# Performance work log

Hardware: AMD Instinct MI355X
Metric: run time of the kernel (lower is better)

The kernel has to match this reference:

```python
import jax, jax.numpy as jnp
import numpy as np

CTX, SP, HIST, NC = 168, 24, 336, 128
LAGS = [24, 48, 72, 96, 120, 144, 168, 0]  # lags_seq + [0]
NSEG = CTX // SP  # 7


def gru_cell(x, h, Wih, Whh, bih, bhh):
    # torch.nn.GRUCell math; x: (N, D), h: (N, H)
    gi = x @ Wih.T + bih
    gh = h @ Whh.T + bhh
    ir, iz, inn = jnp.split(gi, 3, axis=-1)
    hr, hz, hn = jnp.split(gh, 3, axis=-1)
    r = jax.nn.sigmoid(ir + hr)
    z = jax.nn.sigmoid(iz + hz)
    n = jnp.tanh(inn + r * hn)
    return (1.0 - z) * n + z * h


def lstm(x, h, c, Wih, Whh, b):
    # single-layer batch_first LSTM; x: (B, T, D); torch gate order i,f,g,o
    xw = jnp.einsum('btd,gd->btg', x, Wih) + b  # precompute input projection
    def step(carry, xt):
        h, c = carry
        gates = xt + h @ Whh.T
        i, f, g, o = jnp.split(gates, 4, axis=-1)
        c = jax.nn.sigmoid(f) * c + jax.nn.sigmoid(i) * jnp.tanh(g)
        h = jax.nn.sigmoid(o) * jnp.tanh(c)
        return (h, c), h
    (h, c), ys = jax.lax.scan(step, (h, c), jnp.swapaxes(xw, 0, 1))
    return jnp.swapaxes(ys, 0, 1), h, c


def setup_inputs() -> dict:
    key = jax.random.key(0)
    ks = jax.random.split(key, 20)
    B = 8192
    p = lambda k, shape: jax.random.normal(k, shape, jnp.float32) * 0.05
    return dict(
        feat_static_cat=jax.random.randint(ks[0], (B, 1), 0, 50),
        feat_static_real=jax.random.normal(ks[1], (B, 1), jnp.float32),
        past_time_feat=jax.random.normal(ks[2], (B, HIST, 4), jnp.float32),
        past_target=jax.random.uniform(ks[3], (B, HIST), jnp.float32),
        past_observed_values=jnp.ones((B, HIST), jnp.float32),
        future_time_feat=jax.random.normal(ks[4], (B, SP, 4), jnp.float32),
        emb_table=p(ks[5], (50, 16)),
        gru_Wih=p(ks[6], (3 * NC, 30)),
        gru_Whh=p(ks[7], (3 * NC, NC)),
        gru_bih=p(ks[8], (3 * NC,)),
        gru_bhh=p(ks[9], (3 * NC,)),
        enc_Wih=p(ks[10], (NSEG, 4 * NC, NC)),
        enc_Whh=p(ks[11], (NSEG, 4 * NC, NC)),
        enc_b=p(ks[12], (NSEG, 4 * NC)),
        dec_Wih=p(ks[13], (4 * NC, 180)),
        dec_Whh=p(ks[14], (4 * NC, NC)),
        dec_b=p(ks[15], (4 * NC,)),
        out_W=p(ks[16], (1, NC)),
        out_b=p(ks[17], (1,)),
    )


def reference(feat_static_cat, feat_static_real, past_time_feat, past_target,
              past_observed_values, future_time_feat,
              emb_table, gru_Wih, gru_Whh, gru_bih, gru_bhh,
              enc_Wih, enc_Whh, enc_b, dec_Wih, dec_Whh, dec_b,
              out_W, out_b):
    B = past_target.shape[0]
    time_feat = past_time_feat[:, HIST - CTX:, :]  # (B, CTX, 4)

    # lagged subsequences: lagged[:, j, k] = seq[:, HIST - lag_k - CTX + j]
    lags = jnp.stack(
        [past_target[:, HIST - lag - CTX: HIST - lag] for lag in LAGS], axis=-1
    )  # (B, CTX, 8)

    # MeanScaler over past_target[:, CTX:] (keepdim)
    data = past_target[:, CTX:]
    w = past_observed_values[:, CTX:]
    total_w = w.sum(axis=1)                     # (B,)
    wsum = (jnp.abs(data) * w).sum(axis=1)      # (B,)
    default_scale = wsum.sum() / jnp.maximum(total_w.sum(), 1.0)
    scale = wsum / jnp.maximum(total_w, 1.0)
    scale = jnp.maximum(1e-10, jnp.where(wsum > 0, scale, default_scale))
    scale = scale[:, None]                      # (B, 1)

    embedded = emb_table[feat_static_cat[:, 0]]  # (B, 16)
    static_feat = jnp.concatenate([embedded, feat_static_real, jnp.log(scale)], axis=1)  # (B, 18)
    rep_static = jnp.broadcast_to(static_feat[:, None, :], (B, CTX, static_feat.shape[-1]))

    lags_scaled = lags / scale[:, :, None]
    inputs = jnp.concatenate([lags_scaled, time_feat, rep_static], axis=-1)  # (B, CTX, 30)
    inputs = inputs.reshape(B, NSEG, SP, inputs.shape[-1])  # (B, 7, 24, 30)

    encoder_out = jnp.zeros((B, SP, NC), inputs.dtype)
    h = jnp.zeros((B, NC), inputs.dtype)
    c = jnp.zeros((B, NC), inputs.dtype)
    for i in range(NSEG):  # fixed small loop; each segment has distinct LSTM weights
        x = inputs[:, i].reshape(-1, inputs.shape[-1])  # (B*SP, 30)
        hv = gru_cell(x, encoder_out.reshape(-1, NC), gru_Wih, gru_Whh, gru_bih, gru_bhh)
        hv = hv.reshape(B, SP, NC)
        encoder_out, h, c = lstm(hv, h, c, enc_Wih[i], enc_Whh[i], enc_b[i])

    query = jnp.concatenate(
        [inputs[:, 0], encoder_out, future_time_feat, rep_static[:, -SP:, :]], axis=-1
    )  # (B, 24, 180)
    dec_out, _, _ = lstm(query, h, c, dec_Wih, dec_Whh, dec_b)
    outputs = dec_out @ out_W.T + out_b  # (B, 24, 1)
    return outputs * scale[:, :, None]
```

## Files before the change

### kernel.cpp

```cpp
#include <hip/hip_runtime.h>
#include <math.h>

typedef short bf16x8 __attribute__((ext_vector_type(8)));
typedef float f32x4 __attribute__((ext_vector_type(4)));
typedef unsigned short u16;
typedef unsigned int u32;

#define WSUMS 0
#define TOTWS 1
#define WSUM_OFF 2
#define TOTW_OFF 8194
#define SCL_F 16386
#define WB_BYTE 98432

#define GWI_U 0
#define GWH_U 12288
#define EO_U  61440
#define DO_U  978944
#define XG_U  1142784
#define XD_U  23162880

#define L2E 1.4426950408889634f
#define T2E 2.8853900817779268f

__constant__ int cLAG[8] = {144,120,96,72,48,24,0,168};

__device__ __forceinline__ float sig2(float x){
  return __builtin_amdgcn_rcpf(1.0f+__builtin_amdgcn_exp2f(-x));
}
__device__ __forceinline__ float th2(float x){
  return __builtin_fmaf(-2.0f, __builtin_amdgcn_rcpf(__builtin_amdgcn_exp2f(x)+1.0f), 1.0f);
}
__device__ __forceinline__ float thc(float x){
  return th2(x*T2E);
}
__device__ __forceinline__ u16 f2b(float x){ u32 u=__float_as_uint(x); return (u16)((u + 0x7fffu + ((u>>16)&1u))>>16); }
__device__ __forceinline__ float b2f(u16 v){ return __uint_as_float(((u32)v)<<16); }
__device__ __forceinline__ u32 f2b_pk(float lo, float hi){
  u32 r; asm("v_cvt_pk_bf16_f32 %0, %1, %2" : "=v"(r) : "v"(lo), "v"(hi)); return r;
}
__device__ __forceinline__ void pin(bf16x8 &x){
  f32x4 t = __builtin_bit_cast(f32x4, x);
  asm volatile("" : "+v"(t));
  x = __builtin_bit_cast(bf16x8, t);
}

#define MFMA(a,b,c) __builtin_amdgcn_mfma_f32_16x16x32_bf16(a,b,c,0,0,0)

__global__ void scale_kernel(const float* __restrict__ tgt,
                             const float* __restrict__ obs,
                             float* __restrict__ ws)
{
  __shared__ float s1[256], s2[256];
  int b = blockIdx.x*256 + threadIdx.x;
  float wsum=0.f, totw=0.f;
  const float* tr = tgt + b*336 + 168;
  const float* wr = obs + b*336 + 168;
  for(int t=0;t<168;t++){ float w=wr[t]; wsum += fabsf(tr[t])*w; totw += w; }
  ws[WSUM_OFF + b] = wsum;
  ws[TOTW_OFF + b] = totw;
  s1[threadIdx.x]=wsum; s2[threadIdx.x]=totw;
  __syncthreads();
  for(int s=128;s>0;s>>=1){
    if(threadIdx.x<s){ s1[threadIdx.x]+=s1[threadIdx.x+s]; s2[threadIdx.x]+=s2[threadIdx.x+s]; }
    __syncthreads();
  }
  if(threadIdx.x==0){ atomicAdd(&ws[WSUMS], s1[0]); atomicAdd(&ws[TOTWS], s2[0]); }
}

__global__ void prep_w(const float* __restrict__ gWih, const float* __restrict__ gWhh,
                       const float* __restrict__ eWih, const float* __restrict__ eWhh,
                       const float* __restrict__ dWih, const float* __restrict__ dWhh,
                       float* __restrict__ ws)
{
  u16* WU = (u16*)((char*)ws + WB_BYTE);
  int tid = blockIdx.x*blockDim.x + threadIdx.x;
  int nt = gridDim.x*blockDim.x;
  for(int i=tid;i<12288;i+=nt){ int n=i>>5,k=i&31;
    float s=((n>>7)==2)?T2E:L2E;
    WU[GWI_U+i]=(k<30)?f2b(gWih[n*30+k]*s):(u16)0; }
  for(int i=tid;i<49152;i+=nt){ int n=i>>7,k=i&127;
    float s=((n>>7)==2)?T2E:L2E;
    WU[GWH_U+i]=f2b(gWhh[n*128+k]*s); }
  for(int i=tid;i<917504;i+=nt){
    int s=i>>17,r2=i&131071,n=r2>>8,k=r2&255;
    float sc=((n>>7)==2)?T2E:L2E;
    float v=(k<128)?eWih[(s*512+n)*128+k]:eWhh[(s*512+n)*128+(k-128)];
    WU[EO_U+i]=f2b(v*sc);
  }
  for(int i=tid;i<163840;i+=nt){
    int n=i/320, k=i-n*320; float v;
    float sc=((n>>7)==2)?T2E:L2E;
    if(k<128)       v=dWih[n*180+30+k];
    else if(k<136)  v=dWih[n*180+(k-128)];
    else if(k<140)  v=dWih[n*180+8+(k-136)];
    else if(k<144)  v=dWih[n*180+158+(k-140)];
    else if(k<162)  v=dWih[n*180+12+(k-144)];
    else if(k<180)  v=dWih[n*180+162+(k-162)];
    else if(k<192)  v=0.f;
    else            v=dWhh[n*128+(k-192)];
    WU[DO_U+i]=f2b(v*sc);
  }
}

__global__ void prep_x(const float* __restrict__ tgt, const float* __restrict__ ptf,
                       const float* __restrict__ ftf, float* __restrict__ ws)
{
  __shared__ float inv_l[64];
  u16* WU = (u16*)((char*)ws + WB_BYTE);
  const int tid = threadIdx.x;
  const int b0 = blockIdx.x*64;
  if(tid<64){
    int b=b0+tid;
    float wsumv=ws[WSUM_OFF+b], totw=ws[TOTW_OFF+b];
    float def=ws[WSUMS]/fmaxf(ws[TOTWS],1.f);
    float sc=fmaxf(1e-10f,(wsumv>0.f)?wsumv/fmaxf(totw,1.f):def);
    ws[SCL_F+b]=sc; inv_l[tid]=1.f/sc;
  }
  __syncthreads();
  for(int idx=tid; idx<64*168; idx+=256){
    int bl=idx/168, gt=idx-bl*168; int b=b0+bl;
    float iv=inv_l[bl];
    __align__(16) u16 row[16];
    #pragma unroll
    for(int j=0;j<8;j++) row[j]=f2b(tgt[b*336+cLAG[j]+gt]*iv);
    const float* pp=ptf+((size_t)(b*336+168+gt))*4;
    #pragma unroll
    for(int j=0;j<4;j++) row[8+j]=f2b(pp[j]);
    row[12]=row[13]=row[14]=row[15]=0;
    int seg=gt/24, t=gt-seg*24;
    u16* dst=WU+XG_U+(((size_t)seg*8192+b)*24+t)*16;
    *(uint4*)dst=*(const uint4*)row; *(uint4*)(dst+8)=*(const uint4*)(row+8);
  }
  for(int idx=tid; idx<64*24; idx+=256){
    int bl=idx/24, t=idx-bl*24; int b=b0+bl;
    float iv=inv_l[bl];
    __align__(16) u16 row[16];
    #pragma unroll
    for(int j=0;j<8;j++) row[j]=f2b(tgt[b*336+cLAG[j]+t]*iv);
    #pragma unroll
    for(int j=0;j<4;j++) row[8+j]=f2b(ptf[((size_t)(b*336+168+t))*4+j]);
    #pragma unroll
    for(int j=0;j<4;j++) row[12+j]=f2b(ftf[b*96+t*4+j]);
    u16* dst=WU+XD_U+((size_t)b*24+t)*16;
    *(uint4*)dst=*(const uint4*)row; *(uint4*)(dst+8)=*(const uint4*)(row+8);
  }
}

__global__ __launch_bounds__(512,2)
__attribute__((amdgpu_waves_per_eu(2,2)))
void deepar_main(const int* __restrict__ cat, const float* __restrict__ sreal,
                 const float* __restrict__ emb,
                 const float* __restrict__ gbih, const float* __restrict__ gbhh,
                 const float* __restrict__ encb, const float* __restrict__ decb,
                 const float* __restrict__ outW, const float* __restrict__ outb,
                 float* __restrict__ ws, float* __restrict__ out)
{
  asm volatile("" ::: "v252","v253","v254","v255");

  const u16* __restrict__ WU=(const u16*)((const char*)ws+WB_BYTE);

  __shared__ __align__(16) u16 encbuf[384*136];
  __shared__ __align__(16) u16 Ast[2][16*136];
  __shared__ __align__(16) u16 Xast[2][64*40];
  __shared__ __align__(16) u16 Xdast[16*72];
  __shared__ __align__(16) u16 hstash[2][16*136];
  __shared__ u16 statb[16][18];
  __shared__ float scl_s[16];
  __shared__ float outw_s[128];
  __shared__ float red[16][8];
  __shared__ float outb_s;

  const int tid=threadIdx.x;
  const int b0=blockIdx.x*16;
  const int wv=tid>>6, lane=tid&63, quad=lane>>4, l15=lane&15;

  auto stageX = [&](int gc){
    if(tid<128 && gc<42){
      int sg=gc/6, cc=gc-sg*6;
      int a=tid>>1;
      u16* Xb=&Xast[gc&1][0];
      const u16* src=WU+XG_U+(((size_t)sg*8192+b0+(a>>2))*24+4*cc+(a&3))*16;
      if(tid&1) *(uint2*)(Xb+a*40+8)=*(const uint2*)(src+8);
      else      *(uint4*)(Xb+a*40)  =*(const uint4*)src;
    }
  };

  if(tid<16) scl_s[tid]=ws[SCL_F+b0+tid];
  if(tid<128) outw_s[tid]=outW[tid];
  if(tid==128) outb_s=outb[0];
  if(tid>=256){ int q=tid-256; int r=q>>4,k=q&15; statb[r][k]=f2b(emb[cat[b0+r]*16+k]); }
  { const uint4 z4={0,0,0,0};
    for(int i=tid;i<6528;i+=512) *(uint4*)(encbuf+i*8)=z4;
    for(int i=tid;i<544;i+=512)  *(uint4*)(&hstash[0][0]+i*8)=z4;
  }
  __syncthreads();
  if(tid<16){ statb[tid][16]=f2b(sreal[b0+tid]); statb[tid][17]=f2b(logf(scl_s[tid])); }
  __syncthreads();
  for(int i=tid;i<1280;i+=512){ int a=i/20, k=i-a*20+12;
    u16 v=(k<30)?statb[a>>2][k-12]:(u16)0;
    Xast[0][a*40+k]=v; Xast[1][a*40+k]=v; }
  for(int i=tid;i<896;i+=512){ int rr=i/56, k=i-rr*56+16;
    u16 v; if(k<34) v=statb[rr][k-16]; else if(k<52) v=statb[rr][k-34]; else v=0;
    Xdast[rr*72+k]=v; }
  stageX(0);
  __syncthreads();

  float gbi[3], gbh[3];
  #pragma unroll
  for(int j=0;j<3;j++){ int nb=(wv+j*8)*16+l15;
    float s=(j==2)?T2E:L2E;
    gbi[j]=gbih[nb]*s; gbh[j]=gbhh[nb]*s; }
  const float gbr=gbi[0]+gbh[0], gbz=gbi[1]+gbh[1];
  const f32x4 b4r ={gbr,gbr,gbr,gbr};
  const f32x4 b4z ={gbz,gbz,gbz,gbz};
  const f32x4 b4i2={gbi[2],gbi[2],gbi[2],gbi[2]};
  const f32x4 b4h2={gbh[2],gbh[2],gbh[2],gbh[2]};

  float cst[4]={0.f,0.f,0.f,0.f};
  const int hc=wv*16+l15;
  int p=0;

  for(int seg=0;seg<7;seg++){
    bf16x8 gwi[3]; bf16x8 gwh[3][4];
    #pragma unroll
    for(int j=0;j<3;j++){
      int nb=(wv+j*8)*16+l15;
      gwi[j]=*(const bf16x8*)(WU+GWI_U+nb*32+quad*8); pin(gwi[j]);
      #pragma unroll
      for(int kt=0;kt<4;kt++){ gwh[j][kt]=*(const bf16x8*)(WU+GWH_U+nb*128+kt*32+quad*8); pin(gwh[j][kt]); }
    }

    for(int c=0;c<6;c++){
      stageX(seg*6+c+1);
      const u16* Xb = &Xast[c&1][0];

      f32x4 g01[2][4], a2[4], h2[4];
      #pragma unroll
      for(int mt=0;mt<4;mt++){
        bf16x8 af=*(const bf16x8*)(Xb+(mt*16+l15)*40+quad*8);
        g01[0][mt]=MFMA(af,gwi[0],b4r);
        g01[1][mt]=MFMA(af,gwi[1],b4z);
        a2[mt]   =MFMA(af,gwi[2],b4i2);
      }
      const u16* ebase=encbuf+(size_t)(c*64)*136;
      #pragma unroll
      for(int kt=0;kt<4;kt++)
        #pragma unroll
        for(int mt=0;mt<4;mt++){
          bf16x8 af=*(const bf16x8*)(ebase+(mt*16+l15)*136+kt*32+quad*8);
          g01[0][mt]=MFMA(af,gwh[0][kt],g01[0][mt]);
          g01[1][mt]=MFMA(af,gwh[1][kt],g01[1][mt]);
          h2[mt]   =MFMA(af,gwh[2][kt],(kt==0)?b4h2:h2[mt]);
        }
      u16 hv16[4][4];
      #pragma unroll
      for(int mt=0;mt<4;mt++){
        float hv[4];
        #pragma unroll
        for(int reg=0;reg<4;reg++){
          int a=mt*16+quad*4+reg;
          float rg=sig2(g01[0][mt][reg]);
          float zg=sig2(g01[1][mt][reg]);
          float hp=b2f(encbuf[(c*64+a)*136+hc]);
          float nn=th2(__builtin_fmaf(rg,h2[mt][reg],a2[mt][reg]));
          hv[reg]=__builtin_fmaf(zg,hp-nn,nn);
        }
        u32 p01=f2b_pk(hv[0],hv[1]), p23=f2b_pk(hv[2],hv[3]);
        hv16[mt][0]=(u16)p01; hv16[mt][1]=(u16)(p01>>16);
        hv16[mt][2]=(u16)p23; hv16[mt][3]=(u16)(p23>>16);
      }
      __syncthreads();
      #pragma unroll
      for(int mt=0;mt<4;mt++)
        #pragma unroll
        for(int reg=0;reg<4;reg++)
          encbuf[(c*64+mt*16+quad*4+reg)*136+hc]=hv16[mt][reg];
    }

    bf16x8 we[4][8]; f32x4 b4e[4];
    #pragma unroll
    for(int j=0;j<4;j++){
      int nb=(wv+j*8)*16+l15;
      float b=encb[seg*512+nb]*((j==2)?T2E:L2E);
      b4e[j]=(f32x4){b,b,b,b};
      #pragma unroll
      for(int kt=0;kt<8;kt++){
        we[j][kt]=*(const bf16x8*)(WU+EO_U+(size_t)seg*131072+nb*256+kt*32+quad*8);
        pin(we[j][kt]);
      }
    }
    for(int t=0;t<24;t++){
      int tb=(t>>2)*64+(t&3);
      u16* Ab=&Ast[t&1][0];
      if(tid<256){ int row=tid>>4,q=tid&15;
        *(uint4*)(Ab+row*136+q*8)=*(const uint4*)(encbuf+(tb+row*4)*136+q*8); }
      __syncthreads();
      const u16* Hb=&hstash[p][0];
      f32x4 acc[4];
      #pragma unroll
      for(int kt=0;kt<8;kt++){
        bf16x8 af=(kt<4)? *(const bf16x8*)(Ab+l15*136+kt*32+quad*8)
                        : *(const bf16x8*)(Hb+l15*136+(kt-4)*32+quad*8);
        #pragma unroll
        for(int j=0;j<4;j++) acc[j]=MFMA(af,we[j][kt],(kt==0)?b4e[j]:acc[j]);
      }
      u16 hnew[4];
      { float hf[4];
        #pragma unroll
        for(int reg=0;reg<4;reg++){
          float ig=sig2(acc[0][reg]),fg=sig2(acc[1][reg]);
          float gg=th2(acc[2][reg]), og=sig2(acc[3][reg]);
          float c_=__builtin_fmaf(fg,cst[reg],ig*gg); cst[reg]=c_;
          hf[reg]=og*thc(c_);
        }
        u32 p01=f2b_pk(hf[0],hf[1]), p23=f2b_pk(hf[2],hf[3]);
        hnew[0]=(u16)p01; hnew[1]=(u16)(p01>>16);
        hnew[2]=(u16)p23; hnew[3]=(u16)(p23>>16);
      }
      int pn=p^1;
      u16* Hw=&hstash[pn][0];
      #pragma unroll
      for(int reg=0;reg<4;reg++){
        int row=quad*4+reg;
        Hw[row*136+hc]=hnew[reg];
        encbuf[(tb+row*4)*136+hc]=hnew[reg];
      }
      p=pn;
    }
  }

  bf16x8 wd[4][10]; f32x4 b4d[4];
  #pragma unroll
  for(int j=0;j<4;j++){
    int nb=(wv+j*8)*16+l15;
    float b=decb[nb]*((j==2)?T2E:L2E);
    b4d[j]=(f32x4){b,b,b,b};
    #pragma unroll
    for(int kt=0;kt<10;kt++){
      wd[j][kt]=*(const bf16x8*)(WU+DO_U+nb*320+kt*32+quad*8);
      pin(wd[j][kt]);
    }
  }
  for(int t=0;t<24;t++){
    int tb=(t>>2)*64+(t&3);
    u16* Ab=&Ast[t&1][0];
    if(tid<256){ int row=tid>>4,q=tid&15;
      *(uint4*)(Ab+row*136+q*8)=*(const uint4*)(encbuf+(tb+row*4)*136+q*8); }
    else if(tid<288){ int q=tid-256; int rr=q>>1;
      const u16* src=WU+XD_U+((size_t)(b0+rr)*24+t)*16;
      if(q&1) *(uint4*)(Xdast+rr*72+8)=*(const uint4*)(src+8);
      else    *(uint4*)(Xdast+rr*72)  =*(const uint4*)src; }
    __syncthreads();
    const u16* Hb=&hstash[p][0];
    f32x4 acc[4];
    #pragma unroll
    for(int kt=0;kt<10;kt++){
      bf16x8 af=(kt<4)? *(const bf16x8*)(Ab+l15*136+kt*32+quad*8)
              :(kt<6)? *(const bf16x8*)(Xdast+l15*72+(kt-4)*32+quad*8)
                     : *(const bf16x8*)(Hb+l15*136+(kt-6)*32+quad*8);
      #pragma unroll
      for(int j=0;j<4;j++) acc[j]=MFMA(af,wd[j][kt],(kt==0)?b4d[j]:acc[j]);
    }
    u16 hnew[4];
    { float hf[4];
      #pragma unroll
      for(int reg=0;reg<4;reg++){
        float ig=sig2(acc[0][reg]),fg=sig2(acc[1][reg]);
        float gg=th2(acc[2][reg]), og=sig2(acc[3][reg]);
        float c_=__builtin_fmaf(fg,cst[reg],ig*gg); cst[reg]=c_;
        hf[reg]=og*thc(c_);
      }
      u32 p01=f2b_pk(hf[0],hf[1]), p23=f2b_pk(hf[2],hf[3]);
      hnew[0]=(u16)p01; hnew[1]=(u16)(p01>>16);
      hnew[2]=(u16)p23; hnew[3]=(u16)(p23>>16);
    }
    int pn=p^1;
    #pragma unroll
    for(int reg=0;reg<4;reg++)
      hstash[pn][(quad*4+reg)*136+hc]=hnew[reg];
    __syncthreads();
    if(tid<128){ int row=tid>>3,g=tid&7; float s=0.f;
      #pragma unroll
      for(int i=0;i<16;i++) s+=b2f(hstash[pn][row*136+g*16+i])*outw_s[g*16+i];
      red[row][g]=s; }
    __syncthreads();
    if(tid<16){ float s=outb_s;
      #pragma unroll
      for(int g=0;g<8;g++) s+=red[tid][g];
      out[(b0+tid)*24+t]=s*scl_s[tid]; }
    p=pn;
  }
}

extern "C" void kernel_launch(void* const* d_in, const int* in_sizes, int n_in,
                              void* d_out, int out_size, void* d_ws, size_t ws_size,
                              hipStream_t stream)
{
  (void)in_sizes; (void)n_in; (void)out_size; (void)ws_size;
  const int*   cat  = (const int*)d_in[0];
  const float* sreal= (const float*)d_in[1];
  const float* ptf  = (const float*)d_in[2];
  const float* tgt  = (const float*)d_in[3];
  const float* obs  = (const float*)d_in[4];
  const float* ftf  = (const float*)d_in[5];
  const float* emb  = (const float*)d_in[6];
  const float* gWih = (const float*)d_in[7];
  const float* gWhh = (const float*)d_in[8];
  const float* gbih = (const float*)d_in[9];
  const float* gbhh = (const float*)d_in[10];
  const float* eWih = (const float*)d_in[11];
  const float* eWhh = (const float*)d_in[12];
  const float* encb = (const float*)d_in[13];
  const float* dWih = (const float*)d_in[14];
  const float* dWhh = (const float*)d_in[15];
  const float* decb = (const float*)d_in[16];
  const float* outW = (const float*)d_in[17];
  const float* outb = (const float*)d_in[18];
  float* ws  = (float*)d_ws;
  float* out = (float*)d_out;

  hipMemsetAsync(d_ws, 0, 2*sizeof(float), stream);
  scale_kernel<<<dim3(8192/256), dim3(256), 0, stream>>>(tgt, obs, ws);
  prep_w<<<dim3(512), dim3(256), 0, stream>>>(gWih,gWhh,eWih,eWhh,dWih,dWhh,ws);
  prep_x<<<dim3(128), dim3(256), 0, stream>>>(tgt, ptf, ftf, ws);
  deepar_main<<<dim3(512), dim3(512), 0, stream>>>(cat,sreal,emb,gbih,gbhh,encb,decb,
                                                   outW,outb,ws,out);
}
```

Baseline: 939.2 us.

## Precompute next-step input projections and drop LDS staging copies in LSTM loops

The encoder LSTM's input-side MFMAs for step t+1 are now computed during step t, after the recurrent MFMAs, so only the hidden-state half of the product stays on the serial dependency chain. The A-operand staging buffer is removed and rows are read directly from encbuf with a strided address. In the decoder, the per-step global load of future features is double-buffered and issued one step ahead. The X staging ring grows to four slots so it can prefetch two chunks ahead. This adds register pressure from the extra accumulators and reorders the barriers, so correctness depends on the remaining syncthreads protecting hstash and encbuf.

```diff
diff --git a/kernel.cpp b/kernel.cpp
--- a/kernel.cpp
+++ b/kernel.cpp
@@ -161,9 +161,8 @@
   const u16* __restrict__ WU=(const u16*)((const char*)ws+WB_BYTE);
 
   __shared__ __align__(16) u16 encbuf[384*136];
-  __shared__ __align__(16) u16 Ast[2][16*136];
-  __shared__ __align__(16) u16 Xast[2][64*40];
-  __shared__ __align__(16) u16 Xdast[16*72];
+  __shared__ __align__(16) u16 Xast[4][64*40];
+  __shared__ __align__(16) u16 Xdast[2][16*72];
   __shared__ __align__(16) u16 hstash[2][16*136];
   __shared__ u16 statb[16][18];
   __shared__ float scl_s[16];
@@ -179,7 +178,7 @@
     if(tid<128 && gc<42){
       int sg=gc/6, cc=gc-sg*6;
       int a=tid>>1;
-      u16* Xb=&Xast[gc&1][0];
+      u16* Xb=&Xast[gc&3][0];
       const u16* src=WU+XG_U+(((size_t)sg*8192+b0+(a>>2))*24+4*cc+(a&3))*16;
       if(tid&1) *(uint2*)(Xb+a*40+8)=*(const uint2*)(src+8);
       else      *(uint4*)(Xb+a*40)  =*(const uint4*)src;
@@ -199,11 +198,11 @@
   __syncthreads();
   for(int i=tid;i<1280;i+=512){ int a=i/20, k=i-a*20+12;
     u16 v=(k<30)?statb[a>>2][k-12]:(u16)0;
-    Xast[0][a*40+k]=v; Xast[1][a*40+k]=v; }
+    Xast[0][a*40+k]=v; Xast[1][a*40+k]=v; Xast[2][a*40+k]=v; Xast[3][a*40+k]=v; }
   for(int i=tid;i<896;i+=512){ int rr=i/56, k=i-rr*56+16;
     u16 v; if(k<34) v=statb[rr][k-16]; else if(k<52) v=statb[rr][k-34]; else v=0;
-    Xdast[rr*72+k]=v; }
-  stageX(0);
+    Xdast[0][rr*72+k]=v; Xdast[1][rr*72+k]=v; }
+  stageX(0); stageX(1);
   __syncthreads();
 
   float gbi[3], gbh[3];
@@ -232,8 +231,8 @@
     }
 
     for(int c=0;c<6;c++){
-      stageX(seg*6+c+1);
-      const u16* Xb = &Xast[c&1][0];
+      stageX(seg*6+c+2);
+      const u16* Xb = &Xast[(seg*6+c)&3][0];
 
       f32x4 g01[2][4], a2[4], h2[4];
       #pragma unroll
@@ -290,20 +289,35 @@
         pin(we[j][kt]);
       }
     }
+    f32x4 accA[4];
+    {
+      const u16* Ar=encbuf+(size_t)(l15*4)*136;
+      #pragma unroll
+      for(int kt=0;kt<4;kt++){
+        bf16x8 af=*(const bf16x8*)(Ar+kt*32+quad*8);
+        #pragma unroll
+        for(int j=0;j<4;j++) accA[j]=MFMA(af,we[j][kt],(kt==0)?b4e[j]:accA[j]);
+      }
+    }
     for(int t=0;t<24;t++){
-      int tb=(t>>2)*64+(t&3);
-      u16* Ab=&Ast[t&1][0];
-      if(tid<256){ int row=tid>>4,q=tid&15;
-        *(uint4*)(Ab+row*136+q*8)=*(const uint4*)(encbuf+(tb+row*4)*136+q*8); }
       __syncthreads();
       const u16* Hb=&hstash[p][0];
       f32x4 acc[4];
       #pragma unroll
-      for(int kt=0;kt<8;kt++){
-        bf16x8 af=(kt<4)? *(const bf16x8*)(Ab+l15*136+kt*32+quad*8)
-                        : *(const bf16x8*)(Hb+l15*136+(kt-4)*32+quad*8);
-        #pragma unroll
-        for(int j=0;j<4;j++) acc[j]=MFMA(af,we[j][kt],(kt==0)?b4e[j]:acc[j]);
+      for(int kt=0;kt<4;kt++){
+        bf16x8 af=*(const bf16x8*)(Hb+l15*136+kt*32+quad*8);
+        #pragma unroll
+        for(int j=0;j<4;j++) acc[j]=MFMA(af,we[j][kt+4],(kt==0)?accA[j]:acc[j]);
+      }
+      if(t<23){
+        int tb1=((t+1)>>2)*64+((t+1)&3);
+        const u16* Ar=encbuf+(size_t)(tb1+l15*4)*136;
+        #pragma unroll
+        for(int kt=0;kt<4;kt++){
+          bf16x8 af=*(const bf16x8*)(Ar+kt*32+quad*8);
+          #pragma unroll
+          for(int j=0;j<4;j++) accA[j]=MFMA(af,we[j][kt],(kt==0)?b4e[j]:accA[j]);
+        }
       }
       u16 hnew[4];
       { float hf[4];
@@ -319,6 +333,7 @@
         hnew[2]=(u16)p23; hnew[3]=(u16)(p23>>16);
       }
       int pn=p^1;
+      int tb=(t>>2)*64+(t&3);
       u16* Hw=&hstash[pn][0];
       #pragma unroll
       for(int reg=0;reg<4;reg++){
@@ -342,26 +357,31 @@
       pin(wd[j][kt]);
     }
   }
+  if(tid>=256 && tid<288){ int q=tid-256; int rr=q>>1;
+    const u16* src=WU+XD_U+((size_t)(b0+rr)*24+0)*16;
+    u16* Xw=&Xdast[0][0];
+    if(q&1) *(uint4*)(Xw+rr*72+8)=*(const uint4*)(src+8);
+    else    *(uint4*)(Xw+rr*72)  =*(const uint4*)src; }
+  __syncthreads();
   for(int t=0;t<24;t++){
     int tb=(t>>2)*64+(t&3);
-    u16* Ab=&Ast[t&1][0];
-    if(tid<256){ int row=tid>>4,q=tid&15;
-      *(uint4*)(Ab+row*136+q*8)=*(const uint4*)(encbuf+(tb+row*4)*136+q*8); }
-    else if(tid<288){ int q=tid-256; int rr=q>>1;
-      const u16* src=WU+XD_U+((size_t)(b0+rr)*24+t)*16;
-      if(q&1) *(uint4*)(Xdast+rr*72+8)=*(const uint4*)(src+8);
-      else    *(uint4*)(Xdast+rr*72)  =*(const uint4*)src; }
-    __syncthreads();
+    const u16* Ar=encbuf+(size_t)(tb+l15*4)*136;
+    const u16* Xd=&Xdast[t&1][0];
     const u16* Hb=&hstash[p][0];
     f32x4 acc[4];
     #pragma unroll
     for(int kt=0;kt<10;kt++){
-      bf16x8 af=(kt<4)? *(const bf16x8*)(Ab+l15*136+kt*32+quad*8)
-              :(kt<6)? *(const bf16x8*)(Xdast+l15*72+(kt-4)*32+quad*8)
+      bf16x8 af=(kt<4)? *(const bf16x8*)(Ar+kt*32+quad*8)
+              :(kt<6)? *(const bf16x8*)(Xd+l15*72+(kt-4)*32+quad*8)
                      : *(const bf16x8*)(Hb+l15*136+(kt-6)*32+quad*8);
       #pragma unroll
       for(int j=0;j<4;j++) acc[j]=MFMA(af,wd[j][kt],(kt==0)?b4d[j]:acc[j]);
     }
+    if(t<23 && tid>=256 && tid<288){ int q=tid-256; int rr=q>>1;
+      const u16* src=WU+XD_U+((size_t)(b0+rr)*24+t+1)*16;
+      u16* Xw=&Xdast[(t+1)&1][0];
+      if(q&1) *(uint4*)(Xw+rr*72+8)=*(const uint4*)(src+8);
+      else    *(uint4*)(Xw+rr*72)  =*(const uint4*)src; }
     u16 hnew[4];
     { float hf[4];
       #pragma unroll
```

New measurement: 952.3 us. Within noise of the previous version (+1.4%).
